# Performance work log

Hardware: AMD Instinct MI355X
Metric: run time of the kernel (lower is better)

The kernel has to match this reference:

```python
import jax, jax.numpy as jnp
import numpy as np

N = 10000
E = 160000
F_IN = 2000
HID = 128
NC = 5


def setup_inputs() -> dict:
    key = jax.random.key(0)
    ks = jax.random.split(key, 16)
    s = 0.05
    nrm = lambda k, shape: jax.random.normal(k, shape, jnp.float32) * s
    return {
        "x": jax.random.normal(ks[0], (N, F_IN), jnp.float32),
        "edge_index": jax.random.randint(ks[1], (2, E), 0, N),
        # GATConv 1: in=F_IN, out=HID, heads=6, concat=False
        "W_gat1": nrm(ks[2], (F_IN, 6 * HID)), "a_src1": nrm(ks[3], (6, HID)),
        "a_dst1": nrm(ks[4], (6, HID)), "b_gat1": jnp.zeros(HID, jnp.float32),
        # GCNConv 1
        "W_gcn1": nrm(ks[5], (HID, HID)), "b_gcn1": jnp.zeros(HID, jnp.float32),
        # GATConv 2: heads=4
        "W_gat2": nrm(ks[6], (HID, 4 * HID)), "a_src2": nrm(ks[7], (4, HID)),
        "a_dst2": nrm(ks[8], (4, HID)), "b_gat2": jnp.zeros(HID, jnp.float32),
        # GCNConv 2: out=HID//2
        "W_gcn2": nrm(ks[9], (HID, HID // 2)), "b_gcn2": jnp.zeros(HID // 2, jnp.float32),
        # skip projection / fusion
        "W_skip": nrm(ks[10], (F_IN, HID // 2)), "b_skip": jnp.zeros(HID // 2, jnp.float32),
        "W_fuse": nrm(ks[11], (HID + HID // 2, HID // 2)), "b_fuse": jnp.zeros(HID // 2, jnp.float32),
        # classifier MLP
        "W_c1": nrm(ks[12], (HID // 2, HID // 4)), "b_c1": jnp.zeros(HID // 4, jnp.float32),
        "W_c2": nrm(ks[13], (HID // 4, HID // 8)), "b_c2": jnp.zeros(HID // 8, jnp.float32),
        "W_c3": nrm(ks[14], (HID // 8, NC)), "b_c3": jnp.zeros(NC, jnp.float32),
        # LayerNorms
        "g1": jnp.ones(HID, jnp.float32), "be1": jnp.zeros(HID, jnp.float32),
        "g2": jnp.ones(HID, jnp.float32), "be2": jnp.zeros(HID, jnp.float32),
        "g3": jnp.ones(HID // 2, jnp.float32), "be3": jnp.zeros(HID // 2, jnp.float32),
    }


def layer_norm(x, g, b, eps=1e-5):
    mu = jnp.mean(x, axis=-1, keepdims=True)
    var = jnp.var(x, axis=-1, keepdims=True)
    return (x - mu) * jax.lax.rsqrt(var + eps) * g + b


def gat_conv(x, src, dst, W, a_src, a_dst, b, n):
    # PyG GATConv with concat=False (head-mean). Eval mode -> no attn dropout.
    H, C = a_src.shape
    h = (x @ W).reshape(-1, H, C)                      # [N,H,C]
    alpha = (h * a_src).sum(-1)[src] + (h * a_dst).sum(-1)[dst]  # [E,H]
    alpha = jax.nn.leaky_relu(alpha, 0.2)
    m = jax.ops.segment_max(alpha, dst, num_segments=n)
    e = jnp.exp(alpha - m[dst])
    w = e / jax.ops.segment_sum(e, dst, num_segments=n)[dst]     # segment softmax over incoming edges
    out = jax.ops.segment_sum(h[src] * w[:, :, None], dst, num_segments=n)  # [N,H,C]
    return out.mean(axis=1) + b


def gcn_conv(x, src, dst, W, b, n):
    deg = jax.ops.segment_sum(jnp.ones_like(dst, x.dtype), dst, num_segments=n)
    dinv = jnp.where(deg > 0, deg ** -0.5, 0.0)
    msg = (x @ W)[src] * (dinv[src] * dinv[dst])[:, None]
    return jax.ops.segment_sum(msg, dst, num_segments=n) + b


def reference(x, edge_index, W_gat1, a_src1, a_dst1, b_gat1, W_gcn1, b_gcn1,
              W_gat2, a_src2, a_dst2, b_gat2, W_gcn2, b_gcn2,
              W_skip, b_skip, W_fuse, b_fuse, W_c1, b_c1, W_c2, b_c2, W_c3, b_c3,
              g1, be1, g2, be2, g3, be3):
    n = x.shape[0]
    loop = jnp.arange(n, dtype=edge_index.dtype)
    src = jnp.concatenate([edge_index[0], loop])  # add_self_loops
    dst = jnp.concatenate([edge_index[1], loop])

    x1_gat = jax.nn.relu(layer_norm(gat_conv(x, src, dst, W_gat1, a_src1, a_dst1, b_gat1, n), g1, be1))
    x1_gcn = jax.nn.relu(gcn_conv(x1_gat, src, dst, W_gcn1, b_gcn1, n))
    x2_gat = jax.nn.relu(layer_norm(gat_conv(x1_gcn, src, dst, W_gat2, a_src2, a_dst2, b_gat2, n), g2, be2))
    x2_gcn = jax.nn.relu(gcn_conv(x2_gat, src, dst, W_gcn2, b_gcn2, n))

    skip = jax.nn.relu(x @ W_skip + b_skip)
    fused = jax.nn.relu(jnp.concatenate([x1_gcn, x2_gcn], axis=1) @ W_fuse + b_fuse)
    final = layer_norm(fused + skip, g3, be3)

    h = jax.nn.relu(final @ W_c1 + b_c1)
    h = jax.nn.relu(h @ W_c2 + b_c2)
    return h @ W_c3 + b_c3
```

## Files before the change

kernel.cpp:

```cpp
#include <hip/hip_runtime.h>
#include <cstdint>
#include <cstddef>

#define NN 10000
#define NE 160000
#define ET (NE + NN)
#define FIN 2000
#define MPAD 10112
#define KPAD 2048
#define NPAD 896

typedef __bf16 bf16x8 __attribute__((ext_vector_type(8)));
typedef __bf16 bf16x4 __attribute__((ext_vector_type(4)));
typedef float  f32x4  __attribute__((ext_vector_type(4)));

#define GLL(src, dst) __builtin_amdgcn_global_load_lds( \
    (const __attribute__((address_space(1))) void*)(src), \
    (__attribute__((address_space(3))) void*)(dst), 16, 0, 0)

__device__ __forceinline__ void edge_sd(const int* ei, int e, int& s, int& d) {
    if (e < NE) { s = ei[e]; d = ei[NE + e]; }
    else        { s = e - NE; d = e - NE; }
}

__global__ void scan_kernel(const int* deg, int* rowstart, float* dinv) {
    __shared__ int partial[256];
    const int T = 256;
    int chunk = (NN + T - 1) / T;
    int t = threadIdx.x;
    int begin = t * chunk;
    int end = begin + chunk; if (end > NN) end = NN;
    int s = 0;
    for (int i = begin; i < end && i >= begin; i++) s += deg[i];
    partial[t] = s;
    __syncthreads();
    if (t == 0) {
        int run = 0;
        for (int i = 0; i < T; i++) { int v = partial[i]; partial[i] = run; run += v; }
    }
    __syncthreads();
    int run = partial[t];
    for (int i = begin; i < end && i >= begin; i++) {
        rowstart[i] = run; run += deg[i];
        int dg = deg[i];
        dinv[i] = dg > 0 ? rsqrtf((float)dg) : 0.f;
    }
    if (end == NN && begin <= NN) rowstart[NN] = run;
}

__global__ void scatter_kernel(const int* ei, const int* rowstart, int* cursor,
                               int* csr_src) {
    int e = blockIdx.x * blockDim.x + threadIdx.x;
    if (e >= ET) return;
    int s, d; edge_sd(ei, e, s, d);
    int pos = atomicAdd(&cursor[d], 1);
    csr_src[rowstart[d] + pos] = s;
}

#define NBX (158 * 32)
#define NW1 (NPAD * KPAD / 8)
#define NWT (NW1 + 512 * 128 / 8)
#define NWT2 (NWT + 2048 + 1024)
#define WBLK ((NWT2 + 255) / 256)
#define EB 665
__global__ void conv_kernel(const float* __restrict__ x, __bf16* __restrict__ xb,
                            const float* __restrict__ Wg, const float* __restrict__ Ws,
                            const float* __restrict__ W2,
                            const float* __restrict__ Wg1, const float* __restrict__ Wg2,
                            __bf16* __restrict__ wt, __bf16* __restrict__ w2t,
                            __bf16* __restrict__ wgcn1s, __bf16* __restrict__ wgcn2s,
                            const int* __restrict__ ei, int* __restrict__ deg) {
    __shared__ __bf16 slab[4096];
    int bid = blockIdx.x;
    int tid = threadIdx.x;
    if (bid < NBX) {
        int rt = bid >> 5, ks = bid & 31;
        int r = tid >> 2;
        int row = rt * 64 + r;
        int c0 = (tid & 3) * 16;
        int kbase = ks * 64;
#pragma unroll
        for (int j = 0; j < 4; j++) {
            int kl = c0 + j * 4;
            int k = kbase + kl;
            bf16x4 o;
            if (row < NN && k + 3 < FIN) {
                float4 v = *(const float4*)(x + (size_t)row * FIN + k);
                o[0] = (__bf16)v.x; o[1] = (__bf16)v.y;
                o[2] = (__bf16)v.z; o[3] = (__bf16)v.w;
            } else {
                o[0] = o[1] = o[2] = o[3] = (__bf16)0.f;
            }
            int p = kl >> 3, off = kl & 7;
            *(bf16x4*)(slab + (p * 64 + r) * 8 + off) = o;
        }
        __syncthreads();
        size_t base = (size_t)(rt * 32 + ks) * 512;
#pragma unroll
        for (int i = 0; i < 2; i++) {
            int c = i * 256 + tid;
            *(bf16x8*)(xb + (base + c) * 8) = *(const bf16x8*)(slab + c * 8);
        }
    } else if (bid < NBX + WBLK) {
        int g = (bid - NBX) * 256 + tid;
        if (g < NW1) {
            int r = g & 127, p = (g >> 7) & 7, ks = (g >> 10) & 31, ct = g >> 15;
            int n = ct * 128 + r;
            int k0 = ks * 64 + p * 8;
            bf16x8 o;
#pragma unroll
            for (int j = 0; j < 8; j++) {
                int k = k0 + j;
                float v = 0.f;
                if (k < FIN) {
                    if (n < 768)      v = Wg[(size_t)k * 768 + n];
                    else if (n < 832) v = Ws[(size_t)k * 64 + (n - 768)];
                }
                o[j] = (__bf16)v;
            }
            *(bf16x8*)(wt + (size_t)g * 8) = o;
        } else if (g < NWT) {
            int g2 = g - NW1;
            int c = g2 & 2047;
            int ct = g2 >> 11;
            int p = c >> 7, r = c & 127;
            int n = ct * 128 + r;
            int k0 = p * 8;
            bf16x8 o;
#pragma unroll
            for (int j = 0; j < 8; j++)
                o[j] = (__bf16)W2[(size_t)(k0 + j) * 512 + n];
            *(bf16x8*)(w2t + (size_t)g2 * 8) = o;
        } else if (g < NWT + 2048) {
            int g3 = g - NWT;
            int p = g3 >> 7, r = g3 & 127;
            bf16x8 o;
#pragma unroll
            for (int j = 0; j < 8; j++)
                o[j] = (__bf16)Wg1[(size_t)(p * 8 + j) * 128 + r];
            *(bf16x8*)(wgcn1s + (size_t)g3 * 8) = o;
        } else if (g < NWT2) {
            int g4 = g - NWT - 2048;
            int p = g4 >> 6, r = g4 & 63;
            bf16x8 o;
#pragma unroll
            for (int j = 0; j < 8; j++)
                o[j] = (__bf16)Wg2[(size_t)(p * 8 + j) * 64 + r];
            *(bf16x8*)(wgcn2s + (size_t)g4 * 8) = o;
        }
    } else {
        int e = (bid - NBX - WBLK) * 256 + tid;
        if (e < ET) {
            int s, d; edge_sd(ei, e, s, d);
            atomicAdd(&deg[d], 1);
        }
    }
}

__global__ __launch_bounds__(512)
void mfma_gemm1_kernel(const __bf16* __restrict__ xb, const __bf16* __restrict__ wt,
                       const float* __restrict__ a_src1, const float* __restrict__ a_dst1,
                       __bf16* __restrict__ h1b, float* __restrict__ skippre,
                       float* __restrict__ asrc, float* __restrict__ adst) {
    __shared__ __bf16 As[8192];
    __shared__ __bf16 Bs[8192];
    __shared__ float sA[128], sD[128];
    __shared__ float asd[256];
    int b = blockIdx.x;
    int xcd = b & 7, j = b >> 3;
    int jq = j / 7;
    int rt = xcd + 8 * jq;
    int ct = j - 7 * jq;
    if (rt >= MPAD / 128) return;
    const int bi = rt * 128;
    const int bn = ct * 128;

    const int tid = threadIdx.x;
    const int lane = tid & 63;
    const int w = tid >> 6;
    const int wm = w >> 1;
    const int wn = w & 1;
    const int q = lane >> 4, m16 = lane & 15;

    if (tid < 128) { sA[tid] = 0.f; sD[tid] = 0.f; }
    if (ct < 6) {
        if (tid < 128)      asd[tid] = a_src1[ct * 128 + tid];
        else if (tid < 256) asd[tid] = a_dst1[ct * 128 + (tid - 128)];
    }

    f32x4 acc[2][4] = {};

    for (int ks = 0; ks < KPAD / 64; ks++) {
        const size_t slabA = ((size_t)(rt * 2) * 32 + ks) * 512;
        const size_t slabB = ((size_t)ct * 32 + ks) * 1024;
#pragma unroll
        for (int i = 0; i < 2; i++) {
            int seg = i * 8 + w;
            int p = seg >> 1, h = seg & 1;
            GLL(xb + (slabA + (size_t)h * 16384 + p * 64 + lane) * 8,
                As + seg * 512);
        }
#pragma unroll
        for (int i = 0; i < 2; i++) {
            int seg = i * 8 + w;
            GLL(wt + (slabB + seg * 64 + lane) * 8, Bs + seg * 512);
        }
        __syncthreads();

#pragma unroll
        for (int kk = 0; kk < 2; kk++) {
            const int pb = kk * 4 + q;
            bf16x8 af[2], bfr[4];
#pragma unroll
            for (int mt = 0; mt < 2; mt++)
                af[mt] = *(const bf16x8*)(As + (pb * 128 + wm * 32 + mt * 16 + m16) * 8);
#pragma unroll
            for (int nt = 0; nt < 4; nt++)
                bfr[nt] = *(const bf16x8*)(Bs + (pb * 128 + wn * 64 + nt * 16 + m16) * 8);
#pragma unroll
            for (int mt = 0; mt < 2; mt++)
#pragma unroll
                for (int nt = 0; nt < 4; nt++)
                    acc[mt][nt] = __builtin_amdgcn_mfma_f32_16x16x32_bf16(af[mt], bfr[nt], acc[mt][nt], 0, 0, 0);
        }
        __syncthreads();
    }

#pragma unroll
    for (int mt = 0; mt < 2; mt++) {
#pragma unroll
        for (int r = 0; r < 4; r++) {
            int rowl = wm * 32 + mt * 16 + q * 4 + r;
            int row = bi + rowl;
            float ps = 0.f, pd = 0.f;
#pragma unroll
            for (int nt = 0; nt < 4; nt++) {
                int coll = wn * 64 + nt * 16 + m16;
                int col = bn + coll;
                float v = acc[mt][nt][r];
                if (ct < 6) { ps += v * asd[coll]; pd += v * asd[128 + coll]; }
                if (row < NN) {
                    if (col < 768)      h1b[(size_t)row * 768 + col] = (__bf16)v;
                    else if (col < 832) skippre[(size_t)row * 64 + (col - 768)] = v;
                }
            }
            if (ct < 6) {
#pragma unroll
                for (int off = 1; off < 16; off <<= 1) {
                    ps += __shfl_xor(ps, off);
                    pd += __shfl_xor(pd, off);
                }
                if (m16 == 0) { atomicAdd(&sA[rowl], ps); atomicAdd(&sD[rowl], pd); }
            }
        }
    }
    if (ct < 6) {
        __syncthreads();
        if (tid < 128) {
            int row = bi + tid;
            if (row < NN) { asrc[row * 6 + ct] = sA[tid]; adst[row * 6 + ct] = sD[tid]; }
        }
    }
}

__global__ __launch_bounds__(256)
void mfma_gemm2_kernel(const __bf16* __restrict__ A, const __bf16* __restrict__ B,
                       const float* __restrict__ a_src2, const float* __restrict__ a_dst2,
                       __bf16* __restrict__ h2b,
                       float* __restrict__ asrc, float* __restrict__ adst) {
    __shared__ __bf16 As[4096];
    __shared__ __bf16 Bs[8192];
    __shared__ float sA[64], sD[64];
    __shared__ float asd[256];
    const int rt = blockIdx.y, ct = blockIdx.x;
    const int bi = rt * 64, bn = ct * 128;
    const int tid = threadIdx.x, lane = tid & 63, w = tid >> 6;
    const int wm = w >> 1, wn = w & 1;
    const int q = lane >> 4, m16 = lane & 15;

    if (tid < 64) { sA[tid] = 0.f; sD[tid] = 0.f; }
    if (tid < 128) asd[tid] = a_src2[ct * 128 + tid];
    else           asd[tid] = a_dst2[ct * 128 + (tid - 128)];

    f32x4 acc[2][4] = {};

    for (int ks = 0; ks < 2; ks++) {
        const size_t slabA = (size_t)rt * 1024 + ks * 512;
        const size_t slabB = (size_t)ct * 2048 + ks * 1024;
#pragma unroll
        for (int i = 0; i < 2; i++) {
            int seg = i * 4 + w;
            GLL(A + (slabA + seg * 64 + lane) * 8, As + seg * 512);
        }
#pragma unroll
        for (int i = 0; i < 4; i++) {
            int seg = i * 4 + w;
            GLL(B + (slabB + seg * 64 + lane) * 8, Bs + seg * 512);
        }
        __syncthreads();

#pragma unroll
        for (int kk = 0; kk < 2; kk++) {
            const int pb = kk * 4 + q;
            bf16x8 af[2], bfr[4];
#pragma unroll
            for (int mt = 0; mt < 2; mt++)
                af[mt] = *(const bf16x8*)(As + (pb * 64 + wm * 32 + mt * 16 + m16) * 8);
#pragma unroll
            for (int nt = 0; nt < 4; nt++)
                bfr[nt] = *(const bf16x8*)(Bs + (pb * 128 + wn * 64 + nt * 16 + m16) * 8);
#pragma unroll
            for (int mt = 0; mt < 2; mt++)
#pragma unroll
                for (int nt = 0; nt < 4; nt++)
                    acc[mt][nt] = __builtin_amdgcn_mfma_f32_16x16x32_bf16(af[mt], bfr[nt], acc[mt][nt], 0, 0, 0);
        }
        __syncthreads();
    }

#pragma unroll
    for (int mt = 0; mt < 2; mt++) {
#pragma unroll
        for (int r = 0; r < 4; r++) {
            int rowl = wm * 32 + mt * 16 + q * 4 + r;
            int row = bi + rowl;
            float ps = 0.f, pd = 0.f;
#pragma unroll
            for (int nt = 0; nt < 4; nt++) {
                int coll = wn * 64 + nt * 16 + m16;
                float v = acc[mt][nt][r];
                ps += v * asd[coll]; pd += v * asd[128 + coll];
                if (row < NN) h2b[(size_t)row * 512 + bn + coll] = (__bf16)v;
            }
#pragma unroll
            for (int off = 1; off < 16; off <<= 1) {
                ps += __shfl_xor(ps, off);
                pd += __shfl_xor(pd, off);
            }
            if (m16 == 0) { atomicAdd(&sA[rowl], ps); atomicAdd(&sD[rowl], pd); }
        }
    }
    __syncthreads();
    if (tid < 64) {
        int row = bi + tid;
        if (row < NN) { asrc[row * 4 + ct] = sA[tid]; adst[row * 4 + ct] = sD[tid]; }
    }
}

template<int NT>
__global__ __launch_bounds__(256)
void mfma_gcn_kernel(const __bf16* __restrict__ A, const __bf16* __restrict__ B,
                     __bf16* __restrict__ Cb) {
    __shared__ __bf16 As[4096];
    __shared__ __bf16 Bs[NT * 64];
    const int rt = blockIdx.x;
    const int bi = rt * 64;
    const int tid = threadIdx.x, lane = tid & 63, w = tid >> 6;
    const int q = lane >> 4, m16 = lane & 15;
    constexpr int MT = (NT == 128) ? 2 : 1;
    constexpr int MSPAN = (NT == 128) ? 32 : 16;
    const int wm = (NT == 128) ? (w >> 1) : w;
    const int wn = (NT == 128) ? (w & 1) : 0;

    f32x4 acc[MT][4] = {};

    for (int ks = 0; ks < 2; ks++) {
        const size_t slabA = (size_t)rt * 1024 + ks * 512;
        const size_t slabB = (size_t)ks * (NT * 8);
#pragma unroll
        for (int i = 0; i < 2; i++) {
            int seg = i * 4 + w;
            GLL(A + (slabA + seg * 64 + lane) * 8, As + seg * 512);
        }
#pragma unroll
        for (int i = 0; i < NT / 32; i++) {
            int seg = i * 4 + w;
            GLL(B + (slabB + (size_t)seg * 64 + lane) * 8, Bs + seg * 512);
        }
        __syncthreads();

#pragma unroll
        for (int kk = 0; kk < 2; kk++) {
            const int pb = kk * 4 + q;
            bf16x8 af[MT], bfr[4];
#pragma unroll
            for (int mt = 0; mt < MT; mt++)
                af[mt] = *(const bf16x8*)(As + (pb * 64 + wm * MSPAN + mt * 16 + m16) * 8);
#pragma unroll
            for (int nt = 0; nt < 4; nt++)
                bfr[nt] = *(const bf16x8*)(Bs + (pb * NT + wn * 64 + nt * 16 + m16) * 8);
#pragma unroll
            for (int mt = 0; mt < MT; mt++)
#pragma unroll
                for (int nt = 0; nt < 4; nt++)
                    acc[mt][nt] = __builtin_amdgcn_mfma_f32_16x16x32_bf16(af[mt], bfr[nt], acc[mt][nt], 0, 0, 0);
        }
        __syncthreads();
    }

#pragma unroll
    for (int mt = 0; mt < MT; mt++) {
#pragma unroll
        for (int r = 0; r < 4; r++) {
            int row = bi + wm * MSPAN + mt * 16 + q * 4 + r;
            if (row >= NN) continue;
#pragma unroll
            for (int nt = 0; nt < 4; nt++) {
                int col = wn * 64 + nt * 16 + m16;
                Cb[(size_t)row * NT + col] = (__bf16)acc[mt][nt][r];
            }
        }
    }
}

template<int H>
__global__ void gat_agg_kernel(const __bf16* __restrict__ hb,
                               const float* __restrict__ asrc,
                               const float* __restrict__ adst,
                               const int* __restrict__ rowstart,
                               const int* __restrict__ csr_src,
                               const float* __restrict__ bias,
                               const float* __restrict__ gamma,
                               const float* __restrict__ beta,
                               __bf16* __restrict__ outs) {
    constexpr int CH = H * 128;
    constexpr int CAP = 128;
    int n = blockIdx.x;
    int t = threadIdx.x;
    int w = t >> 6, l = t & 63;
    __shared__ float invden[H];
    __shared__ float denp[256];
    __shared__ int   srcs[CAP];
    __shared__ float evs[CAP * H];
    __shared__ float sm[4 * CH];
    __shared__ float red[8];

    int s0 = rowstart[n];
    int deg = rowstart[n + 1] - s0;
    float adst_n = (l < H) ? adst[n * H + l] : 0.f;

    const int eh = t >> 3;
    const int hh1 = t & 7;
    float adst_h = (hh1 < H) ? adst[n * H + hh1] : 0.f;
    float dloc = 0.f;
    for (int base = 0; base < deg; base += 32) {
        int idx = base + eh;
        if (idx < deg) {
            int src = csr_src[s0 + idx];
            if (hh1 == 0 && idx < CAP) srcs[idx] = src;
            if (hh1 < H) {
                float al = asrc[src * H + hh1] + adst_h;
                al = al >= 0.f ? al : 0.2f * al;
                float ev = __expf(al);
                dloc += ev;
                if (idx < CAP) evs[idx * H + hh1] = ev;
            }
        }
    }
    denp[t] = dloc;
    __syncthreads();
    if (t < H) {
        float s = 0.f;
#pragma unroll
        for (int g = 0; g < 32; g++) s += denp[g * 8 + t];
        invden[t] = 1.f / s;
    }
    __syncthreads();

    constexpr int NA = (H == 6) ? 12 : 8;
    float acc[NA] = {};
    const int h0 = l >> 4;
    const int h1i = 4 + (l >> 5);
    int degc = deg < CAP ? deg : CAP;
    int idx = w;
    for (; idx + 4 < degc; idx += 8) {
        int src0 = srcs[idx], src1 = srcs[idx + 4];
        float w00 = evs[idx * H + h0];
        float w10 = evs[(idx + 4) * H + h0];
        const __bf16* hp0 = hb + (size_t)src0 * CH;
        const __bf16* hp1 = hb + (size_t)src1 * CH;
        bf16x8 g00 = *(const bf16x8*)(hp0 + l * 8);
        bf16x8 g10 = *(const bf16x8*)(hp1 + l * 8);
#pragma unroll
        for (int jj = 0; jj < 8; jj++)
            acc[jj] += (float)g00[jj] * w00 + (float)g10[jj] * w10;
        if (H == 6) {
            float w01 = evs[idx * H + h1i];
            float w11 = evs[(idx + 4) * H + h1i];
            bf16x4 g01 = *(const bf16x4*)(hp0 + 512 + l * 4);
            bf16x4 g11 = *(const bf16x4*)(hp1 + 512 + l * 4);
#pragma unroll
            for (int jj = 0; jj < 4; jj++)
                acc[8 + jj] += (float)g01[jj] * w01 + (float)g11[jj] * w11;
        }
    }
    if (idx < degc) {
        int src = srcs[idx];
        float w0 = evs[idx * H + h0];
        const __bf16* hp = hb + (size_t)src * CH;
        bf16x8 hv = *(const bf16x8*)(hp + l * 8);
#pragma unroll
        for (int jj = 0; jj < 8; jj++) acc[jj] += (float)hv[jj] * w0;
        if (H == 6) {
            float w1 = evs[idx * H + h1i];
            bf16x4 hv1 = *(const bf16x4*)(hp + 512 + l * 4);
#pragma unroll
            for (int jj = 0; jj < 4; jj++) acc[8 + jj] += (float)hv1[jj] * w1;
        }
    }
    for (int i2 = CAP + w; i2 < deg; i2 += 4) {
        int src = csr_src[s0 + i2];
        float ev = 0.f;
        if (l < H) {
            float al = asrc[src * H + l] + adst_n;
            al = al >= 0.f ? al : 0.2f * al;
            ev = __expf(al);
        }
        const __bf16* hp = hb + (size_t)src * CH;
        float wgt = __shfl(ev, h0);
        bf16x8 hv = *(const bf16x8*)(hp + l * 8);
#pragma unroll
        for (int jj = 0; jj < 8; jj++) acc[jj] += (float)hv[jj] * wgt;
        if (H == 6) {
            float wg1 = __shfl(ev, h1i);
            bf16x4 hv1 = *(const bf16x4*)(hp + 512 + l * 4);
#pragma unroll
            for (int jj = 0; jj < 4; jj++) acc[8 + jj] += (float)hv1[jj] * wg1;
        }
    }

    *(f32x4*)(sm + w * CH + l * 8)     = *(f32x4*)(acc);
    *(f32x4*)(sm + w * CH + l * 8 + 4) = *(f32x4*)(acc + 4);
    if (H == 6)
        *(f32x4*)(sm + w * CH + 512 + l * 4) = *(f32x4*)(acc + 8);
    __syncthreads();

    float v = 0.f;
    if (t < 128) {
#pragma unroll
        for (int hh = 0; hh < H; hh++) {
            float hsum = 0.f;
#pragma unroll
            for (int ww = 0; ww < 4; ww++) hsum += sm[ww * CH + hh * 128 + t];
            v += hsum * invden[hh];
        }
        v = v * (1.f / H) + bias[t];
    }
    float sv = (t < 128) ? v : 0.f;
    float sq = (t < 128) ? v * v : 0.f;
#pragma unroll
    for (int off = 32; off; off >>= 1) {
        sv += __shfl_down(sv, off);
        sq += __shfl_down(sq, off);
    }
    if ((t & 63) == 0) { red[w * 2] = sv; red[w * 2 + 1] = sq; }
    __syncthreads();
    float tot = red[0] + red[2] + red[4] + red[6];
    float tsq = red[1] + red[3] + red[5] + red[7];
    float mu = tot * (1.f / 128.f);
    float var = tsq * (1.f / 128.f) - mu * mu;
    float r = rsqrtf(var + 1e-5f);
    if (t < 128) {
        float o = fmaxf((v - mu) * r * gamma[t] + beta[t], 0.f);
        int rt2 = n >> 6, rr = n & 63, pp = t >> 3, off2 = t & 7;
        outs[((size_t)(rt2 * 16 + pp) * 64 + rr) * 8 + off2] = (__bf16)o;
    }
}

__global__ void gcn_agg_kernel(const __bf16* __restrict__ y, int C,
                               const float* __restrict__ dinv,
                               const int* __restrict__ rowstart,
                               const int* __restrict__ csr_src,
                               const float* __restrict__ bias,
                               float* __restrict__ out, int ldo, int coloff,
                               __bf16* __restrict__ bout) {
    int n = blockIdx.x;
    int t = threadIdx.x;
    float acc = 0.f;
    int s0 = rowstart[n], s1 = rowstart[n + 1];
    for (int s = s0; s < s1; s++) {
        int src = csr_src[s];
        acc += (float)y[(size_t)src * C + t] * dinv[src];
    }
    float v = fmaxf(acc * dinv[n] + bias[t], 0.f);
    out[(size_t)n * ldo + coloff + t] = v;
    if (bout) {
        int rt = n >> 6, r = n & 63, p = t >> 3, off = t & 7;
        bout[((size_t)(rt * 16 + p) * 64 + r) * 8 + off] = (__bf16)v;
    }
}

__global__ __launch_bounds__(256)
void fuse_final_kernel(const float* __restrict__ cat,
                       const float* __restrict__ skippre,
                       const float* __restrict__ Wf, const float* __restrict__ bfz,
                       const float* __restrict__ b_skip,
                       const float* __restrict__ g3, const float* __restrict__ be3,
                       const float* __restrict__ Wc1, const float* __restrict__ bc1,
                       const float* __restrict__ Wc2, const float* __restrict__ bc2,
                       const float* __restrict__ Wc3, const float* __restrict__ bc3,
                       float* __restrict__ out) {
    __shared__ float WfS[192 * 64];
    __shared__ float catS[4][196];
    __shared__ float fS[4][64], h1S[4][32], h2S[4][16];
    int tid = threadIdx.x;
    int w = tid >> 6, l = tid & 63;
#pragma unroll
    for (int i = 0; i < 12; i++) {
        int idx = (i * 256 + tid) * 4;
        *(f32x4*)(WfS + idx) = *(const f32x4*)(Wf + idx);
    }
    int n = blockIdx.x * 4 + w;
    bool act = n < NN;
    float sk = 0.f;
    if (act) {
        catS[w][l]       = cat[(size_t)n * 192 + l];
        catS[w][64 + l]  = cat[(size_t)n * 192 + 64 + l];
        catS[w][128 + l] = cat[(size_t)n * 192 + 128 + l];
        sk = fmaxf(skippre[(size_t)n * 64 + l] + b_skip[l], 0.f);
    }
    __syncthreads();

    float fu = bfz[l];
#pragma unroll 4
    for (int k = 0; k < 192; k++)
        fu += catS[w][k] * WfS[k * 64 + l];
    float v = fmaxf(fu, 0.f) + sk;

    float sv = v, sq = v * v;
#pragma unroll
    for (int off = 32; off; off >>= 1) {
        sv += __shfl_xor(sv, off);
        sq += __shfl_xor(sq, off);
    }
    float mu = sv * (1.f / 64.f);
    float var = sq * (1.f / 64.f) - mu * mu;
    float r = rsqrtf(var + 1e-5f);
    fS[w][l] = (v - mu) * r * g3[l] + be3[l];
    __syncthreads();
    if (l < 32) {
        float a = bc1[l];
        for (int i = 0; i < 64; i++) a += fS[w][i] * Wc1[i * 32 + l];
        h1S[w][l] = fmaxf(a, 0.f);
    }
    __syncthreads();
    if (l < 16) {
        float a = bc2[l];
        for (int i = 0; i < 32; i++) a += h1S[w][i] * Wc2[i * 16 + l];
        h2S[w][l] = fmaxf(a, 0.f);
    }
    __syncthreads();
    if (l < 5 && act) {
        float a = bc3[l];
        for (int i = 0; i < 16; i++) a += h2S[w][i] * Wc3[i * 5 + l];
        out[(size_t)n * 5 + l] = a;
    }
}

extern "C" void kernel_launch(void* const* d_in, const int* in_sizes, int n_in,
                              void* d_out, int out_size, void* d_ws, size_t ws_size,
                              hipStream_t stream) {
    const float* x      = (const float*)d_in[0];
    const int*   ei     = (const int*)d_in[1];
    const float* W_gat1 = (const float*)d_in[2];
    const float* a_src1 = (const float*)d_in[3];
    const float* a_dst1 = (const float*)d_in[4];
    const float* b_gat1 = (const float*)d_in[5];
    const float* W_gcn1 = (const float*)d_in[6];
    const float* b_gcn1 = (const float*)d_in[7];
    const float* W_gat2 = (const float*)d_in[8];
    const float* a_src2 = (const float*)d_in[9];
    const float* a_dst2 = (const float*)d_in[10];
    const float* b_gat2 = (const float*)d_in[11];
    const float* W_gcn2 = (const float*)d_in[12];
    const float* b_gcn2 = (const float*)d_in[13];
    const float* W_skip = (const float*)d_in[14];
    const float* b_skip = (const float*)d_in[15];
    const float* W_fuse = (const float*)d_in[16];
    const float* b_fuse = (const float*)d_in[17];
    const float* W_c1   = (const float*)d_in[18];
    const float* b_c1   = (const float*)d_in[19];
    const float* W_c2   = (const float*)d_in[20];
    const float* b_c2   = (const float*)d_in[21];
    const float* W_c3   = (const float*)d_in[22];
    const float* b_c3   = (const float*)d_in[23];
    const float* g1     = (const float*)d_in[24];
    const float* be1    = (const float*)d_in[25];
    const float* g2     = (const float*)d_in[26];
    const float* be2    = (const float*)d_in[27];
    const float* g3     = (const float*)d_in[28];
    const float* be3    = (const float*)d_in[29];
    float* out = (float*)d_out;

    char* p = (char*)d_ws;
    auto alloc = [&](size_t bytes) {
        char* r = p; p += (bytes + 255) & ~(size_t)255; return r;
    };
    __bf16* xb      = (__bf16*)alloc((size_t)MPAD * KPAD * 2);
    __bf16* wt      = (__bf16*)alloc((size_t)NPAD * KPAD * 2);
    __bf16* w2t     = (__bf16*)alloc((size_t)512 * 128 * 2);
    __bf16* wgcn1s  = (__bf16*)alloc((size_t)128 * 128 * 2);
    __bf16* wgcn2s  = (__bf16*)alloc((size_t)64 * 128 * 2);
    __bf16* h1b     = (__bf16*)alloc((size_t)NN * 768 * 2);
    __bf16* h2b     = (__bf16*)alloc((size_t)NN * 512 * 2);
    __bf16* ybufb   = (__bf16*)alloc((size_t)NN * 128 * 2);
    __bf16* x1gatb  = (__bf16*)alloc((size_t)3 * MPAD * 128 * 2);
    __bf16* x1gcnb  = x1gatb + (size_t)MPAD * 128;
    __bf16* x2gatb  = x1gcnb + (size_t)MPAD * 128;
    float* asrc     = (float*)alloc((size_t)NN * 6 * 4);
    float* adst     = (float*)alloc((size_t)NN * 6 * 4);
    int*   deg      = (int*)  alloc((size_t)2 * NN * 4);
    int*   cursor   = deg + NN;
    float* dinv     = (float*)alloc((size_t)NN * 4);
    int*   rowst    = (int*)  alloc((size_t)(NN + 1) * 4);
    int*   csrc     = (int*)  alloc((size_t)ET * 4);
    float* cat      = (float*)alloc((size_t)NN * 192 * 4);
    float* skippre  = (float*)alloc((size_t)NN * 64 * 4);

    hipMemsetAsync(deg, 0, (size_t)2 * NN * 4, stream);
    hipMemsetAsync(x1gatb, 0, (size_t)3 * MPAD * 128 * 2, stream);

    conv_kernel<<<NBX + WBLK + EB, 256, 0, stream>>>(
        x, xb, W_gat1, W_skip, W_gat2, W_gcn1, W_gcn2,
        wt, w2t, wgcn1s, wgcn2s, ei, deg);

    scan_kernel   <<<1, 256, 0, stream>>>(deg, rowst, dinv);
    scatter_kernel<<<EB, 256, 0, stream>>>(ei, rowst, cursor, csrc);

    mfma_gemm1_kernel<<<560, 512, 0, stream>>>(xb, wt, a_src1, a_dst1,
                                               h1b, skippre, asrc, adst);

    gat_agg_kernel<6><<<NN, 256, 0, stream>>>(h1b, asrc, adst, rowst, csrc,
                                              b_gat1, g1, be1, x1gatb);
    mfma_gcn_kernel<128><<<MPAD / 64, 256, 0, stream>>>(x1gatb, wgcn1s, ybufb);
    gcn_agg_kernel<<<NN, 128, 0, stream>>>(ybufb, 128, dinv, rowst, csrc,
                                           b_gcn1, cat, 192, 0, x1gcnb);
    mfma_gemm2_kernel<<<dim3(4, MPAD / 64), 256, 0, stream>>>(
        x1gcnb, w2t, a_src2, a_dst2, h2b, asrc, adst);
    gat_agg_kernel<4><<<NN, 256, 0, stream>>>(h2b, asrc, adst, rowst, csrc,
                                              b_gat2, g2, be2, x2gatb);
    mfma_gcn_kernel<64><<<MPAD / 64, 256, 0, stream>>>(x2gatb, wgcn2s, ybufb);
    gcn_agg_kernel<<<NN, 64, 0, stream>>>(ybufb, 64, dinv, rowst, csrc,
                                          b_gcn2, cat, 192, 128, nullptr);
    fuse_final_kernel<<<(NN + 3) / 4, 256, 0, stream>>>(
        cat, skippre, W_fuse, b_fuse, b_skip, g3, be3,
        W_c1, b_c1, W_c2, b_c2, W_c3, b_c3, out);
}
```

Before: 441.1 us.

## Widen x-to-bf16 conversion blocks to 256-wide K with swizzled LDS staging

The fp32-to-bf16 conversion of x now has each block handle a 64-row by 256-column tile instead of 64 by 64, cutting the block count fourfold. Each thread reads 16 contiguous floats per row, so reads run in longer contiguous segments. An XOR swizzle on the LDS row index avoids bank conflicts when writing the repacked 8-element chunks. The cost is a larger 32 KB LDS buffer, which may lower occupancy for this kernel.

```diff
diff --git a/kernel.cpp b/kernel.cpp
--- a/kernel.cpp
+++ b/kernel.cpp
@@ -57,7 +57,7 @@
     csr_src[rowstart[d] + pos] = s;
 }
 
-#define NBX (158 * 32)
+#define NBX (158 * 8)
 #define NW1 (NPAD * KPAD / 8)
 #define NWT (NW1 + 512 * 128 / 8)
 #define NWT2 (NWT + 2048 + 1024)
@@ -70,36 +70,53 @@
                             __bf16* __restrict__ wt, __bf16* __restrict__ w2t,
                             __bf16* __restrict__ wgcn1s, __bf16* __restrict__ wgcn2s,
                             const int* __restrict__ ei, int* __restrict__ deg) {
-    __shared__ __bf16 slab[4096];
+    __shared__ __bf16 ls[16384];
     int bid = blockIdx.x;
     int tid = threadIdx.x;
     if (bid < NBX) {
-        int rt = bid >> 5, ks = bid & 31;
-        int r = tid >> 2;
-        int row = rt * 64 + r;
-        int c0 = (tid & 3) * 16;
-        int kbase = ks * 64;
-#pragma unroll
-        for (int j = 0; j < 4; j++) {
-            int kl = c0 + j * 4;
-            int k = kbase + kl;
-            bf16x4 o;
-            if (row < NN && k + 3 < FIN) {
-                float4 v = *(const float4*)(x + (size_t)row * FIN + k);
-                o[0] = (__bf16)v.x; o[1] = (__bf16)v.y;
-                o[2] = (__bf16)v.z; o[3] = (__bf16)v.w;
-            } else {
-                o[0] = o[1] = o[2] = o[3] = (__bf16)0.f;
+        int rt = bid >> 3, kb = bid & 7;
+        const int lane16 = tid & 15;
+        const int ksl = lane16 >> 2;
+        const int p0 = (lane16 & 3) * 2;
+        const int rbase = tid >> 4;
+        const int kg0 = kb * 256 + lane16 * 16;
+        const int rsw_x = (p0 & 6) ^ ksl;
+#pragma unroll
+        for (int pass = 0; pass < 4; pass++) {
+            int r = pass * 16 + rbase;
+            int row = rt * 64 + r;
+            bf16x8 v0, v1;
+#pragma unroll
+            for (int j = 0; j < 4; j++) {
+                int k = kg0 + j * 4;
+                f32x4 f;
+                if (row < NN && k + 3 < FIN)
+                    f = *(const f32x4*)(x + (size_t)row * FIN + k);
+                else
+                    f = (f32x4){0.f, 0.f, 0.f, 0.f};
+                int o = (j & 1) * 4;
+                if (j < 2) {
+                    v0[o] = (__bf16)f[0]; v0[o+1] = (__bf16)f[1];
+                    v0[o+2] = (__bf16)f[2]; v0[o+3] = (__bf16)f[3];
+                } else {
+                    v1[o] = (__bf16)f[0]; v1[o+1] = (__bf16)f[1];
+                    v1[o+2] = (__bf16)f[2]; v1[o+3] = (__bf16)f[3];
+                }
             }
-            int p = kl >> 3, off = kl & 7;
-            *(bf16x4*)(slab + (p * 64 + r) * 8 + off) = o;
+            int rsw = r ^ rsw_x;
+            *(bf16x8*)(ls + (((ksl * 8 + p0) * 64 + rsw) * 8))     = v0;
+            *(bf16x8*)(ls + (((ksl * 8 + p0 + 1) * 64 + rsw) * 8)) = v1;
         }
         __syncthreads();
-        size_t base = (size_t)(rt * 32 + ks) * 512;
-#pragma unroll
-        for (int i = 0; i < 2; i++) {
-            int c = i * 256 + tid;
-            *(bf16x8*)(xb + (base + c) * 8) = *(const bf16x8*)(slab + c * 8);
+        size_t cbase = ((size_t)rt * 32 + kb * 4) * 512;
+#pragma unroll
+        for (int i = 0; i < 8; i++) {
+            int g = i * 256 + tid;
+            int ksl2 = g >> 9, rem = g & 511;
+            int p = rem >> 6, rr = rem & 63;
+            int rsw = rr ^ ((p & 6) ^ ksl2);
+            bf16x8 v = *(const bf16x8*)(ls + (((ksl2 * 8 + p) * 64 + rsw) * 8));
+            *(bf16x8*)(xb + (cbase + (size_t)ksl2 * 512 + (p * 64 + rr)) * 8) = v;
         }
     } else if (bid < NBX + WBLK) {
         int g = (bid - NBX) * 256 + tid;
```

After: 430.1 us. -2.5%, faster.

## Fuse fp32-to-bf16 conversion of x into GEMM1 A-tile loads; warp-scan in scan kernel

Applied to the files above, without the earlier changes.

Removes the separate pass that converted x to a bf16 tiled buffer. GEMM1 now reads fp32 x directly, converts it in registers and writes swizzled (XOR) tiles into LDS, so the 80MB fp32 read happens once and the 40MB bf16 write plus re-read go away. Because x is re-read by each of the 7 column tiles, and the loads are synchronous rather than async global-to-LDS, there may be more global traffic and less latency hiding. The scan kernel also swaps its serial single-thread prefix for a wavefront shuffle scan.

```diff
diff --git a/kernel.cpp b/kernel.cpp
--- a/kernel.cpp
+++ b/kernel.cpp
@@ -24,28 +24,32 @@
 }
 
 __global__ void scan_kernel(const int* deg, int* rowstart, float* dinv) {
-    __shared__ int partial[256];
+    __shared__ int wsum[4];
     const int T = 256;
     int chunk = (NN + T - 1) / T;
     int t = threadIdx.x;
     int begin = t * chunk;
     int end = begin + chunk; if (end > NN) end = NN;
+    if (begin > NN) begin = NN;
     int s = 0;
-    for (int i = begin; i < end && i >= begin; i++) s += deg[i];
-    partial[t] = s;
-    __syncthreads();
-    if (t == 0) {
-        int run = 0;
-        for (int i = 0; i < T; i++) { int v = partial[i]; partial[i] = run; run += v; }
-    }
-    __syncthreads();
-    int run = partial[t];
-    for (int i = begin; i < end && i >= begin; i++) {
+    for (int i = begin; i < end; i++) s += deg[i];
+    int inc = s;
+#pragma unroll
+    for (int off = 1; off < 64; off <<= 1) {
+        int u = __shfl_up(inc, off);
+        if ((t & 63) >= off) inc += u;
+    }
+    if ((t & 63) == 63) wsum[t >> 6] = inc;
+    __syncthreads();
+    int woff = 0;
+    for (int wv = 0; wv < (t >> 6); wv++) woff += wsum[wv];
+    int run = woff + inc - s;
+    for (int i = begin; i < end; i++) {
         rowstart[i] = run; run += deg[i];
         int dg = deg[i];
         dinv[i] = dg > 0 ? rsqrtf((float)dg) : 0.f;
     }
-    if (end == NN && begin <= NN) rowstart[NN] = run;
+    if (end == NN) rowstart[NN] = run;
 }
 
 __global__ void scatter_kernel(const int* ei, const int* rowstart, int* cursor,
@@ -57,52 +61,21 @@
     csr_src[rowstart[d] + pos] = s;
 }
 
-#define NBX (158 * 32)
 #define NW1 (NPAD * KPAD / 8)
 #define NWT (NW1 + 512 * 128 / 8)
 #define NWT2 (NWT + 2048 + 1024)
 #define WBLK ((NWT2 + 255) / 256)
 #define EB 665
-__global__ void conv_kernel(const float* __restrict__ x, __bf16* __restrict__ xb,
-                            const float* __restrict__ Wg, const float* __restrict__ Ws,
+__global__ void conv_kernel(const float* __restrict__ Wg, const float* __restrict__ Ws,
                             const float* __restrict__ W2,
                             const float* __restrict__ Wg1, const float* __restrict__ Wg2,
                             __bf16* __restrict__ wt, __bf16* __restrict__ w2t,
                             __bf16* __restrict__ wgcn1s, __bf16* __restrict__ wgcn2s,
                             const int* __restrict__ ei, int* __restrict__ deg) {
-    __shared__ __bf16 slab[4096];
     int bid = blockIdx.x;
     int tid = threadIdx.x;
-    if (bid < NBX) {
-        int rt = bid >> 5, ks = bid & 31;
-        int r = tid >> 2;
-        int row = rt * 64 + r;
-        int c0 = (tid & 3) * 16;
-        int kbase = ks * 64;
-#pragma unroll
-        for (int j = 0; j < 4; j++) {
-            int kl = c0 + j * 4;
-            int k = kbase + kl;
-            bf16x4 o;
-            if (row < NN && k + 3 < FIN) {
-                float4 v = *(const float4*)(x + (size_t)row * FIN + k);
-                o[0] = (__bf16)v.x; o[1] = (__bf16)v.y;
-                o[2] = (__bf16)v.z; o[3] = (__bf16)v.w;
-            } else {
-                o[0] = o[1] = o[2] = o[3] = (__bf16)0.f;
-            }
-            int p = kl >> 3, off = kl & 7;
-            *(bf16x4*)(slab + (p * 64 + r) * 8 + off) = o;
-        }
-        __syncthreads();
-        size_t base = (size_t)(rt * 32 + ks) * 512;
-#pragma unroll
-        for (int i = 0; i < 2; i++) {
-            int c = i * 256 + tid;
-            *(bf16x8*)(xb + (base + c) * 8) = *(const bf16x8*)(slab + c * 8);
-        }
-    } else if (bid < NBX + WBLK) {
-        int g = (bid - NBX) * 256 + tid;
+    if (bid < WBLK) {
+        int g = bid * 256 + tid;
         if (g < NW1) {
             int r = g & 127, p = (g >> 7) & 7, ks = (g >> 10) & 31, ct = g >> 15;
             int n = ct * 128 + r;
@@ -149,7 +122,7 @@
             *(bf16x8*)(wgcn2s + (size_t)g4 * 8) = o;
         }
     } else {
-        int e = (bid - NBX - WBLK) * 256 + tid;
+        int e = (bid - WBLK) * 256 + tid;
         if (e < ET) {
             int s, d; edge_sd(ei, e, s, d);
             atomicAdd(&deg[d], 1);
@@ -158,7 +131,7 @@
 }
 
 __global__ __launch_bounds__(512)
-void mfma_gemm1_kernel(const __bf16* __restrict__ xb, const __bf16* __restrict__ wt,
+void mfma_gemm1_kernel(const float* __restrict__ x, const __bf16* __restrict__ wt,
                        const float* __restrict__ a_src1, const float* __restrict__ a_dst1,
                        __bf16* __restrict__ h1b, float* __restrict__ skippre,
                        float* __restrict__ asrc, float* __restrict__ adst) {
@@ -182,6 +155,12 @@
     const int wn = w & 1;
     const int q = lane >> 4, m16 = lane & 15;
 
+    const int rS = tid >> 2;
+    const int pq = tid & 3;
+    const bool rowok = (bi + rS) < NN;
+    const float* xrow = x + (size_t)(bi + rS) * FIN;
+    const int p0 = pq * 2;
+
     if (tid < 128) { sA[tid] = 0.f; sD[tid] = 0.f; }
     if (ct < 6) {
         if (tid < 128)      asd[tid] = a_src1[ct * 128 + tid];
@@ -191,15 +170,28 @@
     f32x4 acc[2][4] = {};
 
     for (int ks = 0; ks < KPAD / 64; ks++) {
-        const size_t slabA = ((size_t)(rt * 2) * 32 + ks) * 512;
+        {
+            int k0 = ks * 64 + pq * 16;
+            bf16x8 v0, v1;
+#pragma unroll
+            for (int jj = 0; jj < 4; jj++) {
+                int k = k0 + jj * 4;
+                f32x4 f;
+                if (rowok && k + 3 < FIN) f = *(const f32x4*)(xrow + k);
+                else                      f = (f32x4){0.f, 0.f, 0.f, 0.f};
+                int o = (jj & 1) * 4;
+                if (jj < 2) {
+                    v0[o] = (__bf16)f[0]; v0[o+1] = (__bf16)f[1];
+                    v0[o+2] = (__bf16)f[2]; v0[o+3] = (__bf16)f[3];
+                } else {
+                    v1[o] = (__bf16)f[0]; v1[o+1] = (__bf16)f[1];
+                    v1[o+2] = (__bf16)f[2]; v1[o+3] = (__bf16)f[3];
+                }
+            }
+            *(bf16x8*)(As + ((p0 * 128 + (rS ^ p0)) * 8))           = v0;
+            *(bf16x8*)(As + (((p0 + 1) * 128 + (rS ^ (p0 + 1))) * 8)) = v1;
+        }
         const size_t slabB = ((size_t)ct * 32 + ks) * 1024;
-#pragma unroll
-        for (int i = 0; i < 2; i++) {
-            int seg = i * 8 + w;
-            int p = seg >> 1, h = seg & 1;
-            GLL(xb + (slabA + (size_t)h * 16384 + p * 64 + lane) * 8,
-                As + seg * 512);
-        }
 #pragma unroll
         for (int i = 0; i < 2; i++) {
             int seg = i * 8 + w;
@@ -212,8 +204,10 @@
             const int pb = kk * 4 + q;
             bf16x8 af[2], bfr[4];
 #pragma unroll
-            for (int mt = 0; mt < 2; mt++)
-                af[mt] = *(const bf16x8*)(As + (pb * 128 + wm * 32 + mt * 16 + m16) * 8);
+            for (int mt = 0; mt < 2; mt++) {
+                int rowm = wm * 32 + mt * 16 + m16;
+                af[mt] = *(const bf16x8*)(As + (pb * 128 + (rowm ^ pb)) * 8);
+            }
 #pragma unroll
             for (int nt = 0; nt < 4; nt++)
                 bfr[nt] = *(const bf16x8*)(Bs + (pb * 128 + wn * 64 + nt * 16 + m16) * 8);
@@ -696,7 +690,6 @@
     auto alloc = [&](size_t bytes) {
         char* r = p; p += (bytes + 255) & ~(size_t)255; return r;
     };
-    __bf16* xb      = (__bf16*)alloc((size_t)MPAD * KPAD * 2);
     __bf16* wt      = (__bf16*)alloc((size_t)NPAD * KPAD * 2);
     __bf16* w2t     = (__bf16*)alloc((size_t)512 * 128 * 2);
     __bf16* wgcn1s  = (__bf16*)alloc((size_t)128 * 128 * 2);
@@ -720,14 +713,14 @@
     hipMemsetAsync(deg, 0, (size_t)2 * NN * 4, stream);
     hipMemsetAsync(x1gatb, 0, (size_t)3 * MPAD * 128 * 2, stream);
 
-    conv_kernel<<<NBX + WBLK + EB, 256, 0, stream>>>(
-        x, xb, W_gat1, W_skip, W_gat2, W_gcn1, W_gcn2,
+    conv_kernel<<<WBLK + EB, 256, 0, stream>>>(
+        W_gat1, W_skip, W_gat2, W_gcn1, W_gcn2,
         wt, w2t, wgcn1s, wgcn2s, ei, deg);
 
     scan_kernel   <<<1, 256, 0, stream>>>(deg, rowst, dinv);
     scatter_kernel<<<EB, 256, 0, stream>>>(ei, rowst, cursor, csrc);
 
-    mfma_gemm1_kernel<<<560, 512, 0, stream>>>(xb, wt, a_src1, a_dst1,
+    mfma_gemm1_kernel<<<560, 512, 0, stream>>>(x, wt, a_src1, a_dst1,
                                                h1b, skippre, asrc, adst);
 
     gat_agg_kernel<6><<<NN, 256, 0, stream>>>(h1b, asrc, adst, rowst, csrc,
```

After: 467.3 us. 1.06x slower.
